# Performance work log

Hardware: AMD Instinct MI355X
Metric: run time of the kernel (lower is better)

The kernel has to match this reference:

```python
import jax, jax.numpy as jnp
import numpy as np

IN_FEATURES = 4096
OUT_FEATURES = 11008
BATCH = 256


def unpack_i4(q):
    # q: [K//2, N] packed bytes; row 2k = low nibble, row 2k+1 = high nibble
    low = q & 15
    high = (q >> 4) & 15
    # interleave -> [K, N]
    return jnp.stack([low, high], axis=1).reshape(q.shape[0] * 2, q.shape[1])


def setup_inputs() -> dict:
    key = jax.random.key(0)
    k1, k2, k3, k4 = jax.random.split(key, 4)
    x = jax.random.normal(k1, (BATCH, IN_FEATURES), dtype=jnp.float32)
    qweight = jax.random.randint(k2, (IN_FEATURES // 2, OUT_FEATURES), 0, 256, dtype=jnp.int32)
    scales = jax.random.uniform(k3, (OUT_FEATURES,), dtype=jnp.float32)
    zeroes = jax.random.normal(k4, (OUT_FEATURES,), dtype=jnp.float32)
    return {"x": x, "qweight": qweight, "scales": scales, "zeroes": zeroes}


def reference(x, qweight, scales, zeroes):
    # Dequantize: per-output-channel scale/zero over unpacked int4 weights
    w = scales[None, :] * unpack_i4(qweight).astype(jnp.float32) - zeroes[None, :]  # [K, N]
    return x @ w  # [B, N]
```

## Files before the change

### kernel.cpp

```cpp
#include <hip/hip_runtime.h>
#include <stdint.h>

#define K_DIM 4096
#define N_DIM 11008
#define M_DIM 256

typedef uint32_t u32;
using frag_ab = __attribute__((ext_vector_type(8))) short;
using frag_cd = __attribute__((ext_vector_type(4))) float;

typedef __attribute__((address_space(3))) const char lds_cc;

#define DSR128(dst, addr, off)                                       \
    asm volatile("ds_read_b128 %0, %1 offset:" #off                  \
                 : "=&v"(dst) : "v"(addr))
#define DSR32(dst, addr, off)                                        \
    asm volatile("ds_read_b32 %0, %1 offset:" #off                   \
                 : "=&v"(dst) : "v"(addr))
#define LGKM(n) do { asm volatile("s_waitcnt lgkmcnt(" #n ")" ::: "memory"); \
                     __builtin_amdgcn_sched_barrier(0); } while (0)
#define VMW(n) asm volatile("s_waitcnt vmcnt(" #n ")" ::: "memory")

__device__ __forceinline__ u32 f2bf_rn(float f) {
    u32 u = __builtin_bit_cast(u32, f);
    return (u + 0x7FFFu + ((u >> 16) & 1u)) >> 16;
}
__device__ __forceinline__ float bf2f(u32 b) {
    return __builtin_bit_cast(float, b << 16);
}
__device__ __forceinline__ void gll16(const void* g, void* l) {
    __builtin_amdgcn_global_load_lds(
        (const __attribute__((address_space(1))) u32*)g,
        (__attribute__((address_space(3))) u32*)l, 16, 0, 0);
}

#define BFCVT(q) ((u32)((__mul24((int)(q), 0x4004) & 0x003C003C) | 0x42004200))

__global__ __launch_bounds__(256) void prep_kernel(const float* __restrict__ x,
                                                   ushort* __restrict__ xbf,
                                                   float* __restrict__ rowsum) {
    const int row = blockIdx.x;
    const int tid = threadIdx.x;
    const float* xr = x + (size_t)row * K_DIM;
    ushort* br = xbf + (size_t)row * K_DIM;
    float s = 0.0f;
#pragma unroll
    for (int p = 0; p < 4; ++p) {
        int i = p * 1024 + tid * 4;
        float4 v = *reinterpret_cast<const float4*>(xr + i);
        u32 b0 = f2bf_rn(v.x), b1 = f2bf_rn(v.y), b2 = f2bf_rn(v.z), b3 = f2bf_rn(v.w);
        uint2 o;
        o.x = b0 | (b1 << 16);
        o.y = b2 | (b3 << 16);
        *reinterpret_cast<uint2*>(br + i) = o;
        s += bf2f(b0) + bf2f(b1) + bf2f(b2) + bf2f(b3);
    }
#pragma unroll
    for (int off = 32; off > 0; off >>= 1) s += __shfl_down(s, off, 64);
    __shared__ float wsum[4];
    if ((tid & 63) == 0) wsum[tid >> 6] = s;
    __syncthreads();
    if (tid == 0) rowsum[row] = wsum[0] + wsum[1] + wsum[2] + wsum[3];
}

__global__ __launch_bounds__(256, 3) void gemm_kernel(const int* __restrict__ qw,
                                                      const float* __restrict__ scales,
                                                      const float* __restrict__ zeroes,
                                                      const ushort* __restrict__ xbf,
                                                      const float* __restrict__ rowsum,
                                                      float* __restrict__ out,
                                                      ushort* __restrict__ partial,
                                                      int split4) {
    __shared__ uint4 Alds[3][512];
    __shared__ u32   Blds[3][2048];

    const u32* qwu = (const u32*)qw;
    const int tid  = threadIdx.x;
    const int lane = tid & 63;
    const int wid  = tid >> 6;
    const int l4   = lane & 15;
    const int c    = lane >> 4;

    const int orig = blockIdx.x;
    int nb, mb, sp, NTt;
    if (split4) {
        int wg = (orig & 7) * 86 + (orig >> 3);
        nb = wg >> 3; sp = (wg >> 1) & 3; mb = wg & 1; NTt = 32;
    } else {
        nb = orig >> 1; mb = orig & 1; sp = 0; NTt = 128;
    }
    const int n0 = nb * 128;
    const int m0 = mb * 128;
    const int wm = wid >> 1;
    const int wn = wid & 1;

    const ushort* asrc[2];
#pragma unroll
    for (int j = 0; j < 2; ++j)
        asrc[j] = xbf + (size_t)(m0 + j * 64 + wid * 16 + (lane >> 2)) * K_DIM +
                  sp * 1024 + 8 * ((lane & 3) ^ ((lane >> 3) & 3));
    const u32* bsrc[2];
#pragma unroll
    for (int r = 0; r < 2; ++r)
        bsrc[r] = qwu + (size_t)(sp * 512 + r * 8 + wid * 2 + (lane >> 5)) * N_DIM +
                  n0 + 4 * ((lane & 31) ^ (((wid >> 1) & 1) << 2));

    const u32 aoff  = (u32)((wm * 64 + l4) * 64 + ((c ^ ((l4 >> 1) & 3)) << 4));
    const u32 b0off = (u32)((c * 4) * 512 + (wn * 64 + ((c & 1) << 4) + l4) * 4);
    const u32 b1off = (u32)((c * 4) * 512 + (wn * 64 + ((1 ^ (c & 1)) << 4) + l4) * 4);

    frag_cd acc[4][4];
#pragma unroll
    for (int i = 0; i < 4; ++i)
#pragma unroll
        for (int j = 0; j < 4; ++j)
            acc[i][j] = (frag_cd){0.f, 0.f, 0.f, 0.f};

    auto stage = [&](int t, int buf) {
#pragma unroll
        for (int j = 0; j < 2; ++j)
            gll16(asrc[j] + (size_t)t * 32, &Alds[buf][j * 256 + wid * 64]);
#pragma unroll
        for (int r = 0; r < 2; ++r)
            gll16(bsrc[r] + (size_t)t * 16 * N_DIM, &Blds[buf][r * 1024 + wid * 256]);
    };

    auto compute = [&](int buf) {
        lds_cc* Ab = (lds_cc*)&Alds[buf][0];
        lds_cc* Bb = (lds_cc*)&Blds[buf][0];
        frag_ab afr[4];
        DSR128(afr[0], Ab + aoff, 0);
        DSR128(afr[1], Ab + aoff, 1024);
        DSR128(afr[2], Ab + aoff, 2048);
        DSR128(afr[3], Ab + aoff, 3072);
        u32 bq[16];
        DSR32(bq[0],  Bb + b0off, 0);
        DSR32(bq[1],  Bb + b0off, 512);
        DSR32(bq[2],  Bb + b0off, 1024);
        DSR32(bq[3],  Bb + b0off, 1536);
        DSR32(bq[4],  Bb + b1off, 0);
        DSR32(bq[5],  Bb + b1off, 512);
        DSR32(bq[6],  Bb + b1off, 1024);
        DSR32(bq[7],  Bb + b1off, 1536);
        DSR32(bq[8],  Bb + b0off, 128);
        DSR32(bq[9],  Bb + b0off, 640);
        DSR32(bq[10], Bb + b0off, 1152);
        DSR32(bq[11], Bb + b0off, 1664);
        DSR32(bq[12], Bb + b1off, 128);
        DSR32(bq[13], Bb + b1off, 640);
        DSR32(bq[14], Bb + b1off, 1152);
        DSR32(bq[15], Bb + b1off, 1664);
        LGKM(12);
#pragma unroll
        for (int nf = 0; nf < 4; ++nf) {
            union { frag_ab f; u32 u[4]; } bb;
            bb.u[0] = BFCVT(bq[nf * 4 + 0]);
            bb.u[1] = BFCVT(bq[nf * 4 + 1]);
            bb.u[2] = BFCVT(bq[nf * 4 + 2]);
            bb.u[3] = BFCVT(bq[nf * 4 + 3]);
#pragma unroll
            for (int mf = 0; mf < 4; ++mf)
                acc[mf][nf] = __builtin_amdgcn_mfma_f32_16x16x32_bf16(
                    afr[mf], bb.f, acc[mf][nf], 0, 0, 0);
            if (nf == 0)      LGKM(8);
            else if (nf == 1) LGKM(4);
            else if (nf == 2) LGKM(0);
        }
    };

    stage(0, 0);

    int cur = 0;
    for (int t = 0; t < NTt; ++t) {
        int pbuf = cur + 1; if (pbuf >= 3) pbuf -= 3;
        if (t + 1 < NTt) {
            stage(t + 1, pbuf);
            VMW(4);
        } else {
            VMW(0);
        }
        __builtin_amdgcn_s_barrier();
        __builtin_amdgcn_sched_barrier(0);
        compute(cur);
        ++cur; if (cur >= 3) cur -= 3;
    }

    float sc[4], zp[4];
#pragma unroll
    for (int nf = 0; nf < 4; ++nf) {
        int n = n0 + wn * 64 + nf * 16 + l4;
        sc[nf] = scales[n];
        zp[nf] = zeroes[n] + 32.0f * sc[nf];
    }
    if (sp == 0) {
        float rs[4][4];
#pragma unroll
        for (int mf = 0; mf < 4; ++mf)
#pragma unroll
            for (int j = 0; j < 4; ++j)
                rs[mf][j] = rowsum[m0 + wm * 64 + mf * 16 + c * 4 + j];
#pragma unroll
        for (int mf = 0; mf < 4; ++mf)
#pragma unroll
            for (int nf = 0; nf < 4; ++nf)
#pragma unroll
                for (int j = 0; j < 4; ++j) {
                    int m = m0 + wm * 64 + mf * 16 + c * 4 + j;
                    out[(size_t)m * N_DIM + n0 + wn * 64 + nf * 16 + l4] =
                        sc[nf] * acc[mf][nf][j] - zp[nf] * rs[mf][j];
                }
    } else {
        ushort* pb = partial + (size_t)(sp - 1) * M_DIM * N_DIM;
#pragma unroll
        for (int mf = 0; mf < 4; ++mf)
#pragma unroll
            for (int nf = 0; nf < 4; ++nf)
#pragma unroll
                for (int j = 0; j < 4; ++j) {
                    int m = m0 + wm * 64 + mf * 16 + c * 4 + j;
                    pb[(size_t)m * N_DIM + n0 + wn * 64 + nf * 16 + l4] =
                        (ushort)f2bf_rn(sc[nf] * acc[mf][nf][j]);
                }
    }
}

__global__ __launch_bounds__(256) void reduce_kernel(float* __restrict__ out,
                                                     const ushort* __restrict__ partial) {
    const size_t NTOT = (size_t)M_DIM * N_DIM;
    size_t i = ((size_t)blockIdx.x * 256 + threadIdx.x) * 4;
    float4 o = *reinterpret_cast<float4*>(out + i);
    ushort4 a = *reinterpret_cast<const ushort4*>(partial + i);
    ushort4 b = *reinterpret_cast<const ushort4*>(partial + NTOT + i);
    ushort4 d = *reinterpret_cast<const ushort4*>(partial + 2 * NTOT + i);
    o.x += bf2f(a.x) + bf2f(b.x) + bf2f(d.x);
    o.y += bf2f(a.y) + bf2f(b.y) + bf2f(d.y);
    o.z += bf2f(a.z) + bf2f(b.z) + bf2f(d.z);
    o.w += bf2f(a.w) + bf2f(b.w) + bf2f(d.w);
    *reinterpret_cast<float4*>(out + i) = o;
}

extern "C" void kernel_launch(void* const* d_in, const int* in_sizes, int n_in,
                              void* d_out, int out_size, void* d_ws, size_t ws_size,
                              hipStream_t stream) {
    const float* x      = (const float*)d_in[0];
    const int*   qw     = (const int*)d_in[1];
    const float* scales = (const float*)d_in[2];
    const float* zeroes = (const float*)d_in[3];
    float* out = (float*)d_out;

    const size_t XBF_BYTES = (size_t)M_DIM * K_DIM * 2;
    const size_t RS_OFF    = XBF_BYTES;
    const size_t P_OFF     = XBF_BYTES + 4096;
    const size_t P_BYTES   = (size_t)3 * M_DIM * N_DIM * 2;

    ushort* xbf    = (ushort*)d_ws;
    float*  rowsum = (float*)((char*)d_ws + RS_OFF);
    ushort* part   = (ushort*)((char*)d_ws + P_OFF);

    const bool split4 = ws_size >= P_OFF + P_BYTES;

    prep_kernel<<<M_DIM, 256, 0, stream>>>(x, xbf, rowsum);
    if (split4) {
        gemm_kernel<<<688, 256, 0, stream>>>(qw, scales, zeroes, xbf, rowsum,
                                             out, part, 1);
        reduce_kernel<<<(M_DIM * N_DIM) / (256 * 4), 256, 0, stream>>>(out, part);
    } else {
        gemm_kernel<<<172, 256, 0, stream>>>(qw, scales, zeroes, xbf, rowsum,
                                             out, nullptr, 0);
    }
}
```

Measured before the change: 49.14 us.

## Remap weight LDS layout for b128 reads and vectorize epilogue stores

Changes which output columns each lane owns so the packed int4 weights can be read from LDS with four ds_read_b128 instead of sixteen ds_read_b32. The global-to-LDS placement of B is rearranged to match, and the MFMA issue order now goes row fragment by row fragment. Because each lane now owns four contiguous columns, the epilogue loads scales, zeroes and rowsum as float4 and writes output and partials as float4 or ushort4 vectors. The aim is fewer LDS instructions and wider global stores. The new B layout drops the old XOR swizzle, which may bring LDS bank conflicts.

New measurement: 48.43 us (median of 2 runs). No clear change (-1.5%).

```diff
diff --git a/kernel.cpp b/kernel.cpp
--- a/kernel.cpp
+++ b/kernel.cpp
@@ -8,14 +8,12 @@
 typedef uint32_t u32;
 using frag_ab = __attribute__((ext_vector_type(8))) short;
 using frag_cd = __attribute__((ext_vector_type(4))) float;
+using u32x4   = __attribute__((ext_vector_type(4))) uint32_t;
 
 typedef __attribute__((address_space(3))) const char lds_cc;
 
 #define DSR128(dst, addr, off)                                       \
     asm volatile("ds_read_b128 %0, %1 offset:" #off                  \
-                 : "=&v"(dst) : "v"(addr))
-#define DSR32(dst, addr, off)                                        \
-    asm volatile("ds_read_b32 %0, %1 offset:" #off                   \
                  : "=&v"(dst) : "v"(addr))
 #define LGKM(n) do { asm volatile("s_waitcnt lgkmcnt(" #n ")" ::: "memory"); \
                      __builtin_amdgcn_sched_barrier(0); } while (0)
@@ -103,11 +101,10 @@
 #pragma unroll
     for (int r = 0; r < 2; ++r)
         bsrc[r] = qwu + (size_t)(sp * 512 + r * 8 + wid * 2 + (lane >> 5)) * N_DIM +
-                  n0 + 4 * ((lane & 31) ^ (((wid >> 1) & 1) << 2));
-
-    const u32 aoff  = (u32)((wm * 64 + l4) * 64 + ((c ^ ((l4 >> 1) & 3)) << 4));
-    const u32 b0off = (u32)((c * 4) * 512 + (wn * 64 + ((c & 1) << 4) + l4) * 4);
-    const u32 b1off = (u32)((c * 4) * 512 + (wn * 64 + ((1 ^ (c & 1)) << 4) + l4) * 4);
+                  n0 + ((lane >> 4) & 1) * 64 + 4 * (lane & 15);
+
+    const u32 aoff = (u32)((wm * 64 + l4) * 64 + ((c ^ ((l4 >> 1) & 3)) << 4));
+    const u32 boff = (u32)(c * 2048 + wn * 256 + l4 * 16);
 
     frag_cd acc[4][4];
 #pragma unroll
@@ -122,50 +119,52 @@
             gll16(asrc[j] + (size_t)t * 32, &Alds[buf][j * 256 + wid * 64]);
 #pragma unroll
         for (int r = 0; r < 2; ++r)
-            gll16(bsrc[r] + (size_t)t * 16 * N_DIM, &Blds[buf][r * 1024 + wid * 256]);
+            gll16(bsrc[r] + (size_t)t * 16 * N_DIM,
+                  &Blds[buf][(r * 256 + wid * 64) * 4]);
     };
 
     auto compute = [&](int buf) {
         lds_cc* Ab = (lds_cc*)&Alds[buf][0];
         lds_cc* Bb = (lds_cc*)&Blds[buf][0];
+        u32x4 bqp[4];
+        DSR128(bqp[0], Bb + boff, 0);
+        DSR128(bqp[1], Bb + boff, 512);
+        DSR128(bqp[2], Bb + boff, 1024);
+        DSR128(bqp[3], Bb + boff, 1536);
         frag_ab afr[4];
         DSR128(afr[0], Ab + aoff, 0);
         DSR128(afr[1], Ab + aoff, 1024);
         DSR128(afr[2], Ab + aoff, 2048);
         DSR128(afr[3], Ab + aoff, 3072);
-        u32 bq[16];
-        DSR32(bq[0],  Bb + b0off, 0);
-        DSR32(bq[1],  Bb + b0off, 512);
-        DSR32(bq[2],  Bb + b0off, 1024);
-        DSR32(bq[3],  Bb + b0off, 1536);
-        DSR32(bq[4],  Bb + b1off, 0);
-        DSR32(bq[5],  Bb + b1off, 512);
-        DSR32(bq[6],  Bb + b1off, 1024);
-        DSR32(bq[7],  Bb + b1off, 1536);
-        DSR32(bq[8],  Bb + b0off, 128);
-        DSR32(bq[9],  Bb + b0off, 640);
-        DSR32(bq[10], Bb + b0off, 1152);
-        DSR32(bq[11], Bb + b0off, 1664);
-        DSR32(bq[12], Bb + b1off, 128);
-        DSR32(bq[13], Bb + b1off, 640);
-        DSR32(bq[14], Bb + b1off, 1152);
-        DSR32(bq[15], Bb + b1off, 1664);
-        LGKM(12);
-#pragma unroll
-        for (int nf = 0; nf < 4; ++nf) {
-            union { frag_ab f; u32 u[4]; } bb;
-            bb.u[0] = BFCVT(bq[nf * 4 + 0]);
-            bb.u[1] = BFCVT(bq[nf * 4 + 1]);
-            bb.u[2] = BFCVT(bq[nf * 4 + 2]);
-            bb.u[3] = BFCVT(bq[nf * 4 + 3]);
-#pragma unroll
-            for (int mf = 0; mf < 4; ++mf)
-                acc[mf][nf] = __builtin_amdgcn_mfma_f32_16x16x32_bf16(
-                    afr[mf], bb.f, acc[mf][nf], 0, 0, 0);
-            if (nf == 0)      LGKM(8);
-            else if (nf == 1) LGKM(4);
-            else if (nf == 2) LGKM(0);
+        LGKM(4);
+        union { frag_ab f; u32 u[4]; } bb[4];
+#pragma unroll
+        for (int j = 0; j < 4; ++j) {
+            bb[j].u[0] = BFCVT(bqp[0][j]);
+            bb[j].u[1] = BFCVT(bqp[1][j]);
+            bb[j].u[2] = BFCVT(bqp[2][j]);
+            bb[j].u[3] = BFCVT(bqp[3][j]);
         }
+        LGKM(3);
+#pragma unroll
+        for (int j = 0; j < 4; ++j)
+            acc[0][j] = __builtin_amdgcn_mfma_f32_16x16x32_bf16(
+                afr[0], bb[j].f, acc[0][j], 0, 0, 0);
+        LGKM(2);
+#pragma unroll
+        for (int j = 0; j < 4; ++j)
+            acc[1][j] = __builtin_amdgcn_mfma_f32_16x16x32_bf16(
+                afr[1], bb[j].f, acc[1][j], 0, 0, 0);
+        LGKM(1);
+#pragma unroll
+        for (int j = 0; j < 4; ++j)
+            acc[2][j] = __builtin_amdgcn_mfma_f32_16x16x32_bf16(
+                afr[2], bb[j].f, acc[2][j], 0, 0, 0);
+        LGKM(0);
+#pragma unroll
+        for (int j = 0; j < 4; ++j)
+            acc[3][j] = __builtin_amdgcn_mfma_f32_16x16x32_bf16(
+                afr[3], bb[j].f, acc[3][j], 0, 0, 0);
     };
 
     stage(0, 0);
@@ -185,42 +184,43 @@
         ++cur; if (cur >= 3) cur -= 3;
     }
 
-    float sc[4], zp[4];
-#pragma unroll
-    for (int nf = 0; nf < 4; ++nf) {
-        int n = n0 + wn * 64 + nf * 16 + l4;
-        sc[nf] = scales[n];
-        zp[nf] = zeroes[n] + 32.0f * sc[nf];
-    }
+    const int ce = n0 + wn * 64 + 4 * l4;
+    const float4 scv = *reinterpret_cast<const float4*>(&scales[ce]);
+    const float4 zv  = *reinterpret_cast<const float4*>(&zeroes[ce]);
+    const float sc[4] = {scv.x, scv.y, scv.z, scv.w};
+    const float zp[4] = {zv.x + 32.0f * scv.x, zv.y + 32.0f * scv.y,
+                         zv.z + 32.0f * scv.z, zv.w + 32.0f * scv.w};
     if (sp == 0) {
-        float rs[4][4];
-#pragma unroll
-        for (int mf = 0; mf < 4; ++mf)
-#pragma unroll
-            for (int j = 0; j < 4; ++j)
-                rs[mf][j] = rowsum[m0 + wm * 64 + mf * 16 + c * 4 + j];
-#pragma unroll
-        for (int mf = 0; mf < 4; ++mf)
-#pragma unroll
-            for (int nf = 0; nf < 4; ++nf)
-#pragma unroll
-                for (int j = 0; j < 4; ++j) {
-                    int m = m0 + wm * 64 + mf * 16 + c * 4 + j;
-                    out[(size_t)m * N_DIM + n0 + wn * 64 + nf * 16 + l4] =
-                        sc[nf] * acc[mf][nf][j] - zp[nf] * rs[mf][j];
-                }
+#pragma unroll
+        for (int mf = 0; mf < 4; ++mf) {
+            const float4 rs = *reinterpret_cast<const float4*>(
+                &rowsum[m0 + wm * 64 + mf * 16 + c * 4]);
+            const float rsa[4] = {rs.x, rs.y, rs.z, rs.w};
+#pragma unroll
+            for (int jr = 0; jr < 4; ++jr) {
+                int m = m0 + wm * 64 + mf * 16 + c * 4 + jr;
+                float4 o;
+                o.x = sc[0] * acc[mf][0][jr] - zp[0] * rsa[jr];
+                o.y = sc[1] * acc[mf][1][jr] - zp[1] * rsa[jr];
+                o.z = sc[2] * acc[mf][2][jr] - zp[2] * rsa[jr];
+                o.w = sc[3] * acc[mf][3][jr] - zp[3] * rsa[jr];
+                *reinterpret_cast<float4*>(&out[(size_t)m * N_DIM + ce]) = o;
+            }
+        }
     } else {
         ushort* pb = partial + (size_t)(sp - 1) * M_DIM * N_DIM;
 #pragma unroll
         for (int mf = 0; mf < 4; ++mf)
 #pragma unroll
-            for (int nf = 0; nf < 4; ++nf)
-#pragma unroll
-                for (int j = 0; j < 4; ++j) {
-                    int m = m0 + wm * 64 + mf * 16 + c * 4 + j;
-                    pb[(size_t)m * N_DIM + n0 + wn * 64 + nf * 16 + l4] =
-                        (ushort)f2bf_rn(sc[nf] * acc[mf][nf][j]);
-                }
+            for (int jr = 0; jr < 4; ++jr) {
+                int m = m0 + wm * 64 + mf * 16 + c * 4 + jr;
+                ushort4 o;
+                o.x = (ushort)f2bf_rn(sc[0] * acc[mf][0][jr]);
+                o.y = (ushort)f2bf_rn(sc[1] * acc[mf][1][jr]);
+                o.z = (ushort)f2bf_rn(sc[2] * acc[mf][2][jr]);
+                o.w = (ushort)f2bf_rn(sc[3] * acc[mf][3][jr]);
+                *reinterpret_cast<ushort4*>(&pb[(size_t)m * N_DIM + ce]) = o;
+            }
     }
 }
 
```
